# Optimization experiments

Measured on AMD Instinct MI355X. Metric: run time of the kernel, lower is better.

The kernel has to match this reference:

```python
import jax, jax.numpy as jnp
import numpy as np

N = 1_000_000
C_IN = 64
COORD_SHIFT = 1024  # keeps shifted coords non-negative (offsets are small)


def setup_inputs() -> dict:
    key = jax.random.key(0)
    ks = jax.random.split(key, 8)
    feats = jax.random.normal(ks[0], (N, C_IN), dtype=jnp.float32)
    coords = jax.random.randint(ks[1], (N, 4), 0, 2048, dtype=jnp.int32)
    mask = jnp.ones((N,), dtype=bool)
    # Pointwise decoder params per decoder_blocks [(64,32),(32,16),(16,3)], bias=True
    s1, s2, s3 = 1.0 / np.sqrt(C_IN), 1.0 / np.sqrt(32), 1.0 / np.sqrt(16)
    W1 = jax.random.normal(ks[2], (C_IN, 32), dtype=jnp.float32) * s1
    b1 = jnp.zeros((32,), dtype=jnp.float32)
    W2 = jax.random.normal(ks[3], (32, 16), dtype=jnp.float32) * s2
    b2 = jnp.zeros((16,), dtype=jnp.float32)
    W3 = jax.random.normal(ks[4], (16, 3), dtype=jnp.float32) * s3
    b3 = jnp.zeros((3,), dtype=jnp.float32)
    return {"feats": feats, "coords": coords, "mask": mask,
            "W1": W1, "b1": b1, "W2": W2, "b2": b2, "W3": W3, "b3": b3}


def _decode(feats, mask, W1, b1, W2, b2, W3, b3):
    # FeatDecoder reduced to its pointwise (kernel-size-1 equivalent) form.
    h = jax.nn.relu(feats @ W1 + b1)
    h = jax.nn.relu(h @ W2 + b2)
    offsets = h @ W3 + b3  # [N, 3]
    return offsets * mask[:, None].astype(offsets.dtype)


def _revoxelize(offsets, coords):
    # offsets_ = [0 | round(offsets)] added to original coords
    off_i = jnp.round(offsets).astype(jnp.int32)                 # [N,3]
    new_coords = coords.at[:, 1:].add(off_i)                     # [N,4]
    # sphash -> unique -> sphashquery == row-wise unique with inverse map
    shifted = new_coords + COORD_SHIFT                           # non-negative rows
    _, inv = jnp.unique(shifted, axis=0, size=N, fill_value=0,
                        return_inverse=True)                      # inv: [N]
    inv = inv.reshape(-1).astype(jnp.int32)
    # spcount: voxels per cluster
    counts = jax.ops.segment_sum(jnp.ones((N,), jnp.float32), inv, num_segments=N)
    # spvoxelize: per-cluster mean of shifted coords, then .int()
    sums = jax.ops.segment_sum(new_coords.astype(jnp.float32), inv, num_segments=N)
    out_coords = (sums / jnp.maximum(counts, 1.0)[:, None]).astype(jnp.int32)
    return out_coords, inv


def reference(feats, coords, mask, W1, b1, W2, b2, W3, b3):
    offsets = _decode(feats, mask, W1, b1, W2, b2, W3, b3)
    out_coords, inv_map = _revoxelize(offsets, coords)
    return offsets, out_coords, inv_map
```

## Files before the change

kernel.cpp:

```cpp
#include <hip/hip_runtime.h>
#include <hip/hip_bf16.h>
#include <stdint.h>


#define TPB 256
#define NB 139264
#define NCHUNK 544
typedef unsigned long long ull;

__global__ __launch_bounds__(256) void k_mlp(
    const float* __restrict__ feats, const int* __restrict__ coords,
    const unsigned char* __restrict__ mask,
    const float* __restrict__ W1, const float* __restrict__ b1,
    const float* __restrict__ W2, const float* __restrict__ b2,
    const float* __restrict__ W3, const float* __restrict__ b3,
    float* __restrict__ out_off, ull* __restrict__ slots,
    unsigned int* __restrict__ cursor, int n)
{
    __shared__ float sW1[2048];
    __shared__ float sW2[512];
    __shared__ float sW3[48];
    __shared__ float sb1[32];
    __shared__ float sb2[16];
    __shared__ float sb3[3];
    for (int t = threadIdx.x; t < 2048; t += TPB) sW1[t] = W1[t];
    for (int t = threadIdx.x; t < 512;  t += TPB) sW2[t] = W2[t];
    if (threadIdx.x < 48) sW3[threadIdx.x] = W3[threadIdx.x];
    if (threadIdx.x < 32) sb1[threadIdx.x] = b1[threadIdx.x];
    if (threadIdx.x < 16) sb2[threadIdx.x] = b2[threadIdx.x];
    if (threadIdx.x < 3)  sb3[threadIdx.x] = b3[threadIdx.x];
    __syncthreads();

    int i = blockIdx.x * TPB + threadIdx.x;
    if (i >= n) return;

    float h1[32];
    #pragma unroll
    for (int j = 0; j < 32; ++j) h1[j] = 0.0f;
    const float4* f4 = (const float4*)(feats + (size_t)i * 64);
    #pragma unroll
    for (int kc = 0; kc < 16; ++kc) {
        float4 xv = f4[kc];
        #pragma unroll
        for (int d = 0; d < 4; ++d) {
            float x = (d == 0) ? xv.x : (d == 1) ? xv.y : (d == 2) ? xv.z : xv.w;
            const float* wr = &sW1[(kc * 4 + d) * 32];
            #pragma unroll
            for (int j = 0; j < 32; j += 4) {
                float4 w = *(const float4*)(wr + j);
                h1[j + 0] = fmaf(x, w.x, h1[j + 0]);
                h1[j + 1] = fmaf(x, w.y, h1[j + 1]);
                h1[j + 2] = fmaf(x, w.z, h1[j + 2]);
                h1[j + 3] = fmaf(x, w.w, h1[j + 3]);
            }
        }
    }
    #pragma unroll
    for (int j = 0; j < 32; ++j) h1[j] = fmaxf(h1[j] + sb1[j], 0.0f);

    float h2[16];
    #pragma unroll
    for (int j = 0; j < 16; ++j) h2[j] = 0.0f;
    #pragma unroll
    for (int k = 0; k < 32; ++k) {
        float x = h1[k];
        const float* wr = &sW2[k * 16];
        #pragma unroll
        for (int j = 0; j < 16; j += 4) {
            float4 w = *(const float4*)(wr + j);
            h2[j + 0] = fmaf(x, w.x, h2[j + 0]);
            h2[j + 1] = fmaf(x, w.y, h2[j + 1]);
            h2[j + 2] = fmaf(x, w.z, h2[j + 2]);
            h2[j + 3] = fmaf(x, w.w, h2[j + 3]);
        }
    }
    #pragma unroll
    for (int j = 0; j < 16; ++j) h2[j] = fmaxf(h2[j] + sb2[j], 0.0f);

    float o0 = 0.0f, o1 = 0.0f, o2 = 0.0f;
    #pragma unroll
    for (int k = 0; k < 16; ++k) {
        float x = h2[k];
        o0 = fmaf(x, sW3[k * 3 + 0], o0);
        o1 = fmaf(x, sW3[k * 3 + 1], o1);
        o2 = fmaf(x, sW3[k * 3 + 2], o2);
    }
    o0 += sb3[0]; o1 += sb3[1]; o2 += sb3[2];

    float m = mask[i] ? 1.0f : 0.0f;
    o0 *= m; o1 *= m; o2 *= m;
    out_off[(size_t)3 * i + 0] = o0;
    out_off[(size_t)3 * i + 1] = o1;
    out_off[(size_t)3 * i + 2] = o2;

    int4 c = ((const int4*)coords)[i];
    int r1 = (int)rintf(o0), r2 = (int)rintf(o1), r3 = (int)rintf(o2);
    int c1u = c.y + r1, c2u = c.z + r2, c3u = c.w + r3;
    int c1s = min(max(c1u + 1024, 0), 8191);
    int c2s = min(max(c2u + 1024, 0), 8191);
    int c3s = min(max(c3u + 1024, 0), 8191);
    int bin1 = min(max((c1u + 64) >> 5, 0), 67);
    int b = c.x * 68 + bin1;
    ull row39 = ((ull)c1s << 26) | ((ull)c2s << 13) | (ull)c3s;
    ull packed = (row39 << 20) | (ull)(unsigned int)i;
    unsigned int j = atomicAdd(&cursor[b], 1u);
    if (j < 64u) slots[(size_t)b * 64 + j] = packed;
}

__device__ inline ull wave_sort64(ull v, int lane)
{
    #pragma unroll
    for (int k = 2; k <= 64; k <<= 1) {
        #pragma unroll
        for (int j = k >> 1; j > 0; j >>= 1) {
            ull o = __shfl_xor(v, j, 64);
            bool up = ((lane & k) == 0);
            bool lower = ((lane & j) == 0);
            ull mn = (v < o) ? v : o;
            ull mx = (v < o) ? o : v;
            v = (up == lower) ? mn : mx;
        }
    }
    return v;
}

__global__ __launch_bounds__(256) void k_passA(
    const ull* __restrict__ slots, const unsigned int* __restrict__ cursor,
    unsigned int* __restrict__ ucnt)
{
    int lane = threadIdx.x & 63;
    int b = blockIdx.x * 4 + (threadIdx.x >> 6);
    unsigned int cnt = cursor[b];
    if (cnt > 64u) cnt = 64u;
    if (cnt == 0u) { if (lane == 0) ucnt[b] = 0u; return; }
    ull v = (lane < (int)cnt) ? slots[(size_t)b * 64 + lane] : ~0ULL;
    v = wave_sort64(v, lane);
    ull row = v >> 20;
    ull prev = __shfl_up(row, 1, 64);
    bool head = (lane < (int)cnt) && ((lane == 0) || (row != prev));
    ull hm = __ballot(head);
    if (lane == 0) ucnt[b] = (unsigned int)__popcll(hm);
}

__global__ __launch_bounds__(256) void k_scanA(
    const unsigned int* __restrict__ ucnt, unsigned int* __restrict__ lstart,
    unsigned int* __restrict__ chsum)
{
    __shared__ unsigned int s[256];
    int tid = threadIdx.x;
    int g = blockIdx.x * 256 + tid;
    unsigned int v = ucnt[g];
    s[tid] = v;
    __syncthreads();
    for (int ofs = 1; ofs < 256; ofs <<= 1) {
        unsigned int t = (tid >= ofs) ? s[tid - ofs] : 0u;
        __syncthreads();
        s[tid] += t;
        __syncthreads();
    }
    lstart[g] = s[tid] - v;
    if (tid == 255) chsum[blockIdx.x] = s[255];
}

__global__ __launch_bounds__(1024) void k_scanB(unsigned int* __restrict__ chsum)
{
    __shared__ unsigned int s[1024];
    int tid = threadIdx.x;
    unsigned int v = (tid < NCHUNK) ? chsum[tid] : 0u;
    s[tid] = v;
    __syncthreads();
    for (int ofs = 1; ofs < 1024; ofs <<= 1) {
        unsigned int t = (tid >= ofs) ? s[tid - ofs] : 0u;
        __syncthreads();
        s[tid] += t;
        __syncthreads();
    }
    if (tid < NCHUNK) chsum[tid] = s[tid] - v;
}

__global__ __launch_bounds__(256) void k_passB(
    const ull* __restrict__ slots, const unsigned int* __restrict__ cursor,
    const unsigned int* __restrict__ lstart, const unsigned int* __restrict__ chbase,
    float* __restrict__ out_oc, float* __restrict__ out_inv)
{
    int lane = threadIdx.x & 63;
    int b = blockIdx.x * 4 + (threadIdx.x >> 6);
    unsigned int cnt = cursor[b];
    if (cnt > 64u) cnt = 64u;
    if (cnt == 0u) return;
    ull v = (lane < (int)cnt) ? slots[(size_t)b * 64 + lane] : ~0ULL;
    v = wave_sort64(v, lane);
    ull row = v >> 20;
    unsigned int idx = (unsigned int)(v & 0xFFFFFULL);
    ull prev = __shfl_up(row, 1, 64);
    bool head = (lane < (int)cnt) && ((lane == 0) || (row != prev));
    ull hm = __ballot(head);
    ull le = (lane == 63) ? ~0ULL : ((1ULL << (lane + 1)) - 1ULL);
    int lrank = __popcll(hm & le) - 1;
    unsigned int base = chbase[b >> 8] + lstart[b];
    unsigned int r = base + (unsigned int)lrank;
    if (lane < (int)cnt) out_inv[idx] = (float)r;

    int c3s = (int)(row & 0x1FFFULL);
    int c2s = (int)((row >> 13) & 0x1FFFULL);
    int c1s = (int)(row >> 26);
    ull sum = (lane < (int)cnt)
        ? ((1ULL << 57) | ((ull)c1s << 38) | ((ull)c2s << 19) | (ull)c3s)
        : 0ULL;
    ull P = sum;
    #pragma unroll
    for (int d = 1; d < 64; d <<= 1) {
        ull t = __shfl_up(P, d, 64);
        if (lane >= d) P += t;
    }
    ull gt = hm & ~le;
    int tpos = gt ? (__ffsll((long long)gt) - 2) : ((int)cnt - 1);
    ull Pt = __shfl(P, tpos, 64);
    int hsrc = (lane > 0) ? lane - 1 : 0;
    ull Ph = __shfl(P, hsrc, 64);
    if (lane == 0) Ph = 0ULL;
    if (head) {
        ull run = Pt - Ph;
        int rc = (int)(run >> 57);
        int s1 = (int)((run >> 38) & 0x7FFFFULL) - 1024 * rc;
        int s2 = (int)((run >> 19) & 0x7FFFFULL) - 1024 * rc;
        int s3 = (int)(run & 0x7FFFFULL) - 1024 * rc;
        float fc = (float)rc;
        float4 o;
        o.x = (float)((unsigned int)b / 68u);
        o.y = truncf((float)s1 / fc);
        o.z = truncf((float)s2 / fc);
        o.w = truncf((float)s3 / fc);
        ((float4*)out_oc)[r] = o;
    }
}

extern "C" void kernel_launch(void* const* d_in, const int* in_sizes, int n_in,
                              void* d_out, int out_size, void* d_ws, size_t ws_size,
                              hipStream_t stream)
{
    const float*         feats  = (const float*)d_in[0];
    const int*           coords = (const int*)d_in[1];
    const unsigned char* mask   = (const unsigned char*)d_in[2];
    const float* W1 = (const float*)d_in[3];
    const float* b1 = (const float*)d_in[4];
    const float* W2 = (const float*)d_in[5];
    const float* b2 = (const float*)d_in[6];
    const float* W3 = (const float*)d_in[7];
    const float* b3 = (const float*)d_in[8];

    int n = in_sizes[1] / 4;

    char* ws = (char*)d_ws;
    ull*          slots  = (ull*)ws;
    unsigned int* cursor = (unsigned int*)(ws + (size_t)NB * 64 * 8);
    unsigned int* ucnt   = cursor + NB;
    unsigned int* lstart = ucnt + NB;
    unsigned int* chsum  = lstart + NB;

    float* out     = (float*)d_out;
    float* out_off = out;
    float* out_oc  = out + (size_t)3 * n;
    float* out_inv = out + (size_t)7 * n;

    hipMemsetAsync(cursor, 0, (size_t)NB * sizeof(unsigned int), stream);
    hipMemsetAsync(out_oc, 0, (size_t)4 * n * sizeof(float), stream);

    int nb256 = (n + TPB - 1) / TPB;

    k_mlp<<<nb256, TPB, 0, stream>>>(feats, coords, mask, W1, b1, W2, b2, W3, b3,
                                     out_off, slots, cursor, n);
    k_passA<<<NB / 4, TPB, 0, stream>>>(slots, cursor, ucnt);
    k_scanA<<<NCHUNK, 256, 0, stream>>>(ucnt, lstart, chsum);
    k_scanB<<<1, 1024, 0, stream>>>(chsum);
    k_passB<<<NB / 4, TPB, 0, stream>>>(slots, cursor, lstart, chsum, out_oc, out_inv);
}
```

Measured before the change: 599.2 us.

## Use finer 16-slot buckets and precompute ranks and cluster means in passA

The coordinate bucketing moves from 68 bins of width 32 with 64 slots each to 272 bins of width 8 with 16 slots each. Each wavefront now sorts four 16-element segments with a shorter bitonic network. PassA now computes per-point local ranks and per-cluster mean coordinates once and stores them, so passB becomes a cheap scatter that no longer re-sorts. The MLP kernel processes two points per thread so each shared-memory weight load is reused. Risks include bucket overflow past 16 entries in denser bins, more workspace traffic for the stored ranks and means, and higher register pressure in the MLP.

```diff
diff --git a/kernel.cpp b/kernel.cpp
--- a/kernel.cpp
+++ b/kernel.cpp
@@ -4,8 +4,9 @@
 
 
 #define TPB 256
-#define NB 139264
-#define NCHUNK 544
+#define NBINS1 272
+#define NB (2048 * NBINS1)
+#define NCHUNK (NB / 1024)
 typedef unsigned long long ull;
 
 __global__ __launch_bounds__(256) void k_mlp(
@@ -31,135 +32,201 @@
     if (threadIdx.x < 3)  sb3[threadIdx.x] = b3[threadIdx.x];
     __syncthreads();
 
-    int i = blockIdx.x * TPB + threadIdx.x;
-    if (i >= n) return;
-
-    float h1[32];
-    #pragma unroll
-    for (int j = 0; j < 32; ++j) h1[j] = 0.0f;
-    const float4* f4 = (const float4*)(feats + (size_t)i * 64);
-    #pragma unroll
+    int i0 = blockIdx.x * (2 * TPB) + threadIdx.x;
+    int i1 = i0 + TPB;
+    bool va = (i0 < n), vb = (i1 < n);
+    if (!va) return;
+
+    float h1a[32], h1b[32];
+    #pragma unroll
+    for (int j = 0; j < 32; ++j) { h1a[j] = 0.0f; h1b[j] = 0.0f; }
+    const float4* fa = (const float4*)(feats + (size_t)i0 * 64);
+    const float4* fb = (const float4*)(feats + (size_t)i1 * 64);
     for (int kc = 0; kc < 16; ++kc) {
-        float4 xv = f4[kc];
+        float4 xva = fa[kc];
+        float4 xvb = vb ? fb[kc] : make_float4(0.f, 0.f, 0.f, 0.f);
         #pragma unroll
         for (int d = 0; d < 4; ++d) {
-            float x = (d == 0) ? xv.x : (d == 1) ? xv.y : (d == 2) ? xv.z : xv.w;
+            float xA = (d == 0) ? xva.x : (d == 1) ? xva.y : (d == 2) ? xva.z : xva.w;
+            float xB = (d == 0) ? xvb.x : (d == 1) ? xvb.y : (d == 2) ? xvb.z : xvb.w;
             const float* wr = &sW1[(kc * 4 + d) * 32];
             #pragma unroll
             for (int j = 0; j < 32; j += 4) {
                 float4 w = *(const float4*)(wr + j);
-                h1[j + 0] = fmaf(x, w.x, h1[j + 0]);
-                h1[j + 1] = fmaf(x, w.y, h1[j + 1]);
-                h1[j + 2] = fmaf(x, w.z, h1[j + 2]);
-                h1[j + 3] = fmaf(x, w.w, h1[j + 3]);
+                h1a[j + 0] = fmaf(xA, w.x, h1a[j + 0]);
+                h1a[j + 1] = fmaf(xA, w.y, h1a[j + 1]);
+                h1a[j + 2] = fmaf(xA, w.z, h1a[j + 2]);
+                h1a[j + 3] = fmaf(xA, w.w, h1a[j + 3]);
+                h1b[j + 0] = fmaf(xB, w.x, h1b[j + 0]);
+                h1b[j + 1] = fmaf(xB, w.y, h1b[j + 1]);
+                h1b[j + 2] = fmaf(xB, w.z, h1b[j + 2]);
+                h1b[j + 3] = fmaf(xB, w.w, h1b[j + 3]);
             }
         }
     }
     #pragma unroll
-    for (int j = 0; j < 32; ++j) h1[j] = fmaxf(h1[j] + sb1[j], 0.0f);
-
-    float h2[16];
-    #pragma unroll
-    for (int j = 0; j < 16; ++j) h2[j] = 0.0f;
-    #pragma unroll
+    for (int j = 0; j < 32; ++j) {
+        h1a[j] = fmaxf(h1a[j] + sb1[j], 0.0f);
+        h1b[j] = fmaxf(h1b[j] + sb1[j], 0.0f);
+    }
+
+    float h2a[16], h2b[16];
+    #pragma unroll
+    for (int j = 0; j < 16; ++j) { h2a[j] = 0.0f; h2b[j] = 0.0f; }
     for (int k = 0; k < 32; ++k) {
-        float x = h1[k];
+        float xA = h1a[k], xB = h1b[k];
         const float* wr = &sW2[k * 16];
         #pragma unroll
         for (int j = 0; j < 16; j += 4) {
             float4 w = *(const float4*)(wr + j);
-            h2[j + 0] = fmaf(x, w.x, h2[j + 0]);
-            h2[j + 1] = fmaf(x, w.y, h2[j + 1]);
-            h2[j + 2] = fmaf(x, w.z, h2[j + 2]);
-            h2[j + 3] = fmaf(x, w.w, h2[j + 3]);
+            h2a[j + 0] = fmaf(xA, w.x, h2a[j + 0]);
+            h2a[j + 1] = fmaf(xA, w.y, h2a[j + 1]);
+            h2a[j + 2] = fmaf(xA, w.z, h2a[j + 2]);
+            h2a[j + 3] = fmaf(xA, w.w, h2a[j + 3]);
+            h2b[j + 0] = fmaf(xB, w.x, h2b[j + 0]);
+            h2b[j + 1] = fmaf(xB, w.y, h2b[j + 1]);
+            h2b[j + 2] = fmaf(xB, w.z, h2b[j + 2]);
+            h2b[j + 3] = fmaf(xB, w.w, h2b[j + 3]);
         }
     }
     #pragma unroll
-    for (int j = 0; j < 16; ++j) h2[j] = fmaxf(h2[j] + sb2[j], 0.0f);
-
-    float o0 = 0.0f, o1 = 0.0f, o2 = 0.0f;
+    for (int j = 0; j < 16; ++j) {
+        h2a[j] = fmaxf(h2a[j] + sb2[j], 0.0f);
+        h2b[j] = fmaxf(h2b[j] + sb2[j], 0.0f);
+    }
+
+    float oa0 = 0.f, oa1 = 0.f, oa2 = 0.f, ob0 = 0.f, ob1 = 0.f, ob2 = 0.f;
     #pragma unroll
     for (int k = 0; k < 16; ++k) {
-        float x = h2[k];
-        o0 = fmaf(x, sW3[k * 3 + 0], o0);
-        o1 = fmaf(x, sW3[k * 3 + 1], o1);
-        o2 = fmaf(x, sW3[k * 3 + 2], o2);
-    }
-    o0 += sb3[0]; o1 += sb3[1]; o2 += sb3[2];
-
-    float m = mask[i] ? 1.0f : 0.0f;
-    o0 *= m; o1 *= m; o2 *= m;
-    out_off[(size_t)3 * i + 0] = o0;
-    out_off[(size_t)3 * i + 1] = o1;
-    out_off[(size_t)3 * i + 2] = o2;
-
-    int4 c = ((const int4*)coords)[i];
-    int r1 = (int)rintf(o0), r2 = (int)rintf(o1), r3 = (int)rintf(o2);
-    int c1u = c.y + r1, c2u = c.z + r2, c3u = c.w + r3;
-    int c1s = min(max(c1u + 1024, 0), 8191);
-    int c2s = min(max(c2u + 1024, 0), 8191);
-    int c3s = min(max(c3u + 1024, 0), 8191);
-    int bin1 = min(max((c1u + 64) >> 5, 0), 67);
-    int b = c.x * 68 + bin1;
-    ull row39 = ((ull)c1s << 26) | ((ull)c2s << 13) | (ull)c3s;
-    ull packed = (row39 << 20) | (ull)(unsigned int)i;
-    unsigned int j = atomicAdd(&cursor[b], 1u);
-    if (j < 64u) slots[(size_t)b * 64 + j] = packed;
-}
-
-__device__ inline ull wave_sort64(ull v, int lane)
-{
-    #pragma unroll
-    for (int k = 2; k <= 64; k <<= 1) {
+        float xA = h2a[k], xB = h2b[k];
+        float w0 = sW3[k * 3 + 0], w1 = sW3[k * 3 + 1], w2 = sW3[k * 3 + 2];
+        oa0 = fmaf(xA, w0, oa0); oa1 = fmaf(xA, w1, oa1); oa2 = fmaf(xA, w2, oa2);
+        ob0 = fmaf(xB, w0, ob0); ob1 = fmaf(xB, w1, ob1); ob2 = fmaf(xB, w2, ob2);
+    }
+    oa0 += sb3[0]; oa1 += sb3[1]; oa2 += sb3[2];
+    ob0 += sb3[0]; ob1 += sb3[1]; ob2 += sb3[2];
+
+    #pragma unroll
+    for (int r = 0; r < 2; ++r) {
+        int i = r ? i1 : i0;
+        if (r && !vb) break;
+        float o0 = r ? ob0 : oa0, o1 = r ? ob1 : oa1, o2 = r ? ob2 : oa2;
+        float m = mask[i] ? 1.0f : 0.0f;
+        o0 *= m; o1 *= m; o2 *= m;
+        out_off[(size_t)3 * i + 0] = o0;
+        out_off[(size_t)3 * i + 1] = o1;
+        out_off[(size_t)3 * i + 2] = o2;
+
+        int4 c = ((const int4*)coords)[i];
+        int r1 = (int)rintf(o0), r2 = (int)rintf(o1), r3 = (int)rintf(o2);
+        int c1u = c.y + r1, c2u = c.z + r2, c3u = c.w + r3;
+        int c1s = min(max(c1u + 1024, 0), 8191);
+        int c2s = min(max(c2u + 1024, 0), 8191);
+        int c3s = min(max(c3u + 1024, 0), 8191);
+        int bin1 = min(max((c1u + 64) >> 3, 0), NBINS1 - 1);
+        int b = c.x * NBINS1 + bin1;
+        ull row39 = ((ull)c1s << 26) | ((ull)c2s << 13) | (ull)c3s;
+        ull packed = (row39 << 20) | (ull)(unsigned int)i;
+        unsigned int j = atomicAdd(&cursor[b], 1u);
+        if (j < 16u) slots[(size_t)b * 16 + j] = packed;
+    }
+}
+
+__global__ __launch_bounds__(256) void k_passA(
+    const ull* __restrict__ slots, const unsigned int* __restrict__ cursor,
+    unsigned int* __restrict__ ucnt, unsigned int* __restrict__ ptrec,
+    ull* __restrict__ headval)
+{
+    int tid = threadIdx.x;
+    int lane = tid & 63;
+    int wv = tid >> 6;
+    int wb4 = blockIdx.x * 16 + wv * 4;
+    int seg = lane >> 4, sl = lane & 15;
+    int b = wb4 + seg;
+    unsigned int cnt = cursor[b];
+    if (cnt > 16u) cnt = 16u;
+
+    ull v = (sl < (int)cnt) ? slots[(size_t)wb4 * 16 + lane] : ~0ULL;
+
+    #pragma unroll
+    for (int k = 2; k <= 16; k <<= 1) {
         #pragma unroll
         for (int j = k >> 1; j > 0; j >>= 1) {
             ull o = __shfl_xor(v, j, 64);
-            bool up = ((lane & k) == 0);
-            bool lower = ((lane & j) == 0);
+            bool up = ((sl & k) == 0);
+            bool lower = ((sl & j) == 0);
             ull mn = (v < o) ? v : o;
             ull mx = (v < o) ? o : v;
             v = (up == lower) ? mn : mx;
         }
     }
-    return v;
-}
-
-__global__ __launch_bounds__(256) void k_passA(
-    const ull* __restrict__ slots, const unsigned int* __restrict__ cursor,
-    unsigned int* __restrict__ ucnt)
-{
-    int lane = threadIdx.x & 63;
-    int b = blockIdx.x * 4 + (threadIdx.x >> 6);
-    unsigned int cnt = cursor[b];
-    if (cnt > 64u) cnt = 64u;
-    if (cnt == 0u) { if (lane == 0) ucnt[b] = 0u; return; }
-    ull v = (lane < (int)cnt) ? slots[(size_t)b * 64 + lane] : ~0ULL;
-    v = wave_sort64(v, lane);
+
     ull row = v >> 20;
-    ull prev = __shfl_up(row, 1, 64);
-    bool head = (lane < (int)cnt) && ((lane == 0) || (row != prev));
+    unsigned int idx = (unsigned int)(v & 0xFFFFFULL);
+    ull prow = __shfl_up(v, 1, 64) >> 20;
+    bool head = (sl < (int)cnt) && ((sl == 0) || (row != prow));
     ull hm = __ballot(head);
-    if (lane == 0) ucnt[b] = (unsigned int)__popcll(hm);
-}
-
-__global__ __launch_bounds__(256) void k_scanA(
+    unsigned int hseg = (unsigned int)((hm >> (seg * 16)) & 0xFFFFULL);
+    unsigned int le = (2u << sl) - 1u;
+    int lrank = __popc(hseg & le) - 1;
+    if (sl == 0) ucnt[b] = (unsigned int)__popc(hseg);
+    if (sl < (int)cnt)
+        ptrec[(size_t)wb4 * 16 + lane] = (idx << 4) | (unsigned int)lrank;
+
+    int c3s = (int)(row & 0x1FFFULL);
+    int c2s = (int)((row >> 13) & 0x1FFFULL);
+    int c1s = (int)((row >> 26) & 0x1FFFULL);
+    ull sum = (sl < (int)cnt)
+        ? ((1ULL << 57) | ((ull)c1s << 38) | ((ull)c2s << 19) | (ull)c3s)
+        : 0ULL;
+    ull P = sum;
+    #pragma unroll
+    for (int d = 1; d < 16; d <<= 1) {
+        ull t = __shfl_up(P, d, 64);
+        if (sl >= d) P += t;
+    }
+    unsigned int above = hseg & ~le;
+    int tpos = above ? (__ffs(above) - 2) : ((int)cnt - 1);
+    if (tpos < 0) tpos = 0;
+    ull Pt = __shfl(P, seg * 16 + tpos, 64);
+    ull Pp = __shfl_up(P, 1, 64);
+    ull Ph = (sl == 0) ? 0ULL : Pp;
+
+    if (head) {
+        ull run = Pt - Ph;
+        int rc = (int)(run >> 57);
+        int s1 = (int)((run >> 38) & 0x7FFFFULL) - 1024 * rc;
+        int s2 = (int)((run >> 19) & 0x7FFFFULL) - 1024 * rc;
+        int s3 = (int)(run & 0x7FFFFULL) - 1024 * rc;
+        float fc = (float)rc;
+        int m1 = (int)truncf((float)s1 / fc);
+        int m2 = (int)truncf((float)s2 / fc);
+        int m3 = (int)truncf((float)s3 / fc);
+        int c0 = (unsigned int)b / NBINS1;
+        ull hv = ((ull)c0 << 39) | ((ull)(m1 + 1029) << 26) |
+                 ((ull)(m2 + 1029) << 13) | (ull)(m3 + 1029);
+        headval[(size_t)b * 16 + lrank] = hv;
+    }
+}
+
+__global__ __launch_bounds__(1024) void k_scanA(
     const unsigned int* __restrict__ ucnt, unsigned int* __restrict__ lstart,
     unsigned int* __restrict__ chsum)
 {
-    __shared__ unsigned int s[256];
+    __shared__ unsigned int s[1024];
     int tid = threadIdx.x;
-    int g = blockIdx.x * 256 + tid;
+    int g = blockIdx.x * 1024 + tid;
     unsigned int v = ucnt[g];
     s[tid] = v;
     __syncthreads();
-    for (int ofs = 1; ofs < 256; ofs <<= 1) {
+    for (int ofs = 1; ofs < 1024; ofs <<= 1) {
         unsigned int t = (tid >= ofs) ? s[tid - ofs] : 0u;
         __syncthreads();
         s[tid] += t;
         __syncthreads();
     }
     lstart[g] = s[tid] - v;
-    if (tid == 255) chsum[blockIdx.x] = s[255];
+    if (tid == 1023) chsum[blockIdx.x] = s[1023];
 }
 
 __global__ __launch_bounds__(1024) void k_scanB(unsigned int* __restrict__ chsum)
@@ -179,59 +246,29 @@
 }
 
 __global__ __launch_bounds__(256) void k_passB(
-    const ull* __restrict__ slots, const unsigned int* __restrict__ cursor,
+    const unsigned int* __restrict__ cursor, const unsigned int* __restrict__ ucnt,
     const unsigned int* __restrict__ lstart, const unsigned int* __restrict__ chbase,
+    const unsigned int* __restrict__ ptrec, const ull* __restrict__ headval,
     float* __restrict__ out_oc, float* __restrict__ out_inv)
 {
-    int lane = threadIdx.x & 63;
-    int b = blockIdx.x * 4 + (threadIdx.x >> 6);
+    int t = blockIdx.x * TPB + threadIdx.x;
+    int b = t >> 4, sl = t & 15;
+    unsigned int base = chbase[b >> 10] + lstart[b];
     unsigned int cnt = cursor[b];
-    if (cnt > 64u) cnt = 64u;
-    if (cnt == 0u) return;
-    ull v = (lane < (int)cnt) ? slots[(size_t)b * 64 + lane] : ~0ULL;
-    v = wave_sort64(v, lane);
-    ull row = v >> 20;
-    unsigned int idx = (unsigned int)(v & 0xFFFFFULL);
-    ull prev = __shfl_up(row, 1, 64);
-    bool head = (lane < (int)cnt) && ((lane == 0) || (row != prev));
-    ull hm = __ballot(head);
-    ull le = (lane == 63) ? ~0ULL : ((1ULL << (lane + 1)) - 1ULL);
-    int lrank = __popcll(hm & le) - 1;
-    unsigned int base = chbase[b >> 8] + lstart[b];
-    unsigned int r = base + (unsigned int)lrank;
-    if (lane < (int)cnt) out_inv[idx] = (float)r;
-
-    int c3s = (int)(row & 0x1FFFULL);
-    int c2s = (int)((row >> 13) & 0x1FFFULL);
-    int c1s = (int)(row >> 26);
-    ull sum = (lane < (int)cnt)
-        ? ((1ULL << 57) | ((ull)c1s << 38) | ((ull)c2s << 19) | (ull)c3s)
-        : 0ULL;
-    ull P = sum;
-    #pragma unroll
-    for (int d = 1; d < 64; d <<= 1) {
-        ull t = __shfl_up(P, d, 64);
-        if (lane >= d) P += t;
-    }
-    ull gt = hm & ~le;
-    int tpos = gt ? (__ffsll((long long)gt) - 2) : ((int)cnt - 1);
-    ull Pt = __shfl(P, tpos, 64);
-    int hsrc = (lane > 0) ? lane - 1 : 0;
-    ull Ph = __shfl(P, hsrc, 64);
-    if (lane == 0) Ph = 0ULL;
-    if (head) {
-        ull run = Pt - Ph;
-        int rc = (int)(run >> 57);
-        int s1 = (int)((run >> 38) & 0x7FFFFULL) - 1024 * rc;
-        int s2 = (int)((run >> 19) & 0x7FFFFULL) - 1024 * rc;
-        int s3 = (int)(run & 0x7FFFFULL) - 1024 * rc;
-        float fc = (float)rc;
+    if (cnt > 16u) cnt = 16u;
+    if (sl < (int)cnt) {
+        unsigned int rec = ptrec[t];
+        out_inv[rec >> 4] = (float)(base + (rec & 0xFu));
+    }
+    unsigned int u = ucnt[b];
+    if (sl < (int)u) {
+        ull hv = headval[t];
         float4 o;
-        o.x = (float)((unsigned int)b / 68u);
-        o.y = truncf((float)s1 / fc);
-        o.z = truncf((float)s2 / fc);
-        o.w = truncf((float)s3 / fc);
-        ((float4*)out_oc)[r] = o;
+        o.x = (float)(unsigned int)(hv >> 39);
+        o.y = (float)((int)((hv >> 26) & 0x1FFFULL) - 1029);
+        o.z = (float)((int)((hv >> 13) & 0x1FFFULL) - 1029);
+        o.w = (float)((int)(hv & 0x1FFFULL) - 1029);
+        ((float4*)out_oc)[base + sl] = o;
     }
 }
 
@@ -252,11 +289,13 @@
     int n = in_sizes[1] / 4;
 
     char* ws = (char*)d_ws;
-    ull*          slots  = (ull*)ws;
-    unsigned int* cursor = (unsigned int*)(ws + (size_t)NB * 64 * 8);
-    unsigned int* ucnt   = cursor + NB;
-    unsigned int* lstart = ucnt + NB;
-    unsigned int* chsum  = lstart + NB;
+    ull*          slots   = (ull*)ws;
+    ull*          headval = (ull*)(ws + (size_t)NB * 16 * 8);
+    unsigned int* ptrec   = (unsigned int*)(ws + (size_t)NB * 16 * 16);
+    unsigned int* cursor  = ptrec + (size_t)NB * 16;
+    unsigned int* ucnt    = cursor + NB;
+    unsigned int* lstart  = ucnt + NB;
+    unsigned int* chsum   = lstart + NB;
 
     float* out     = (float*)d_out;
     float* out_off = out;
@@ -266,12 +305,13 @@
     hipMemsetAsync(cursor, 0, (size_t)NB * sizeof(unsigned int), stream);
     hipMemsetAsync(out_oc, 0, (size_t)4 * n * sizeof(float), stream);
 
-    int nb256 = (n + TPB - 1) / TPB;
-
-    k_mlp<<<nb256, TPB, 0, stream>>>(feats, coords, mask, W1, b1, W2, b2, W3, b3,
+    int nbMLP = (n + 2 * TPB - 1) / (2 * TPB);
+
+    k_mlp<<<nbMLP, TPB, 0, stream>>>(feats, coords, mask, W1, b1, W2, b2, W3, b3,
                                      out_off, slots, cursor, n);
-    k_passA<<<NB / 4, TPB, 0, stream>>>(slots, cursor, ucnt);
-    k_scanA<<<NCHUNK, 256, 0, stream>>>(ucnt, lstart, chsum);
+    k_passA<<<NB / 16, TPB, 0, stream>>>(slots, cursor, ucnt, ptrec, headval);
+    k_scanA<<<NCHUNK, 1024, 0, stream>>>(ucnt, lstart, chsum);
     k_scanB<<<1, 1024, 0, stream>>>(chsum);
-    k_passB<<<NB / 4, TPB, 0, stream>>>(slots, cursor, lstart, chsum, out_oc, out_inv);
-}
+    k_passB<<<NB / 16, TPB, 0, stream>>>(cursor, ucnt, lstart, chsum, ptrec, headval,
+                                         out_oc, out_inv);
+}
```

New measurement: 665.0 us. +11.0%, slower.
